# Kernel optimization log

Hardware: AMD Instinct MI355X
Metric: run time of the kernel (lower is better)

## Reference

```python
import jax, jax.numpy as jnp
import numpy as np

N_NODES = 100000
N_EDGES = 3200000
IN_CH, HIDDEN, OUT_CH = 256, 16, 16


def setup_inputs() -> dict:
    key = jax.random.key(0)
    k1, k2, k3, k4, k5, k6 = jax.random.split(key, 6)
    x = jax.random.normal(k1, (N_NODES, IN_CH), dtype=jnp.float32)
    edge_index = jax.random.randint(k2, (2, N_EDGES), 0, N_NODES, dtype=jnp.int64)
    W1 = jax.random.normal(k3, (IN_CH, HIDDEN), dtype=jnp.float32) * (1.0 / np.sqrt(IN_CH))
    b1 = jax.random.normal(k4, (HIDDEN,), dtype=jnp.float32) * 0.01
    W2 = jax.random.normal(k5, (HIDDEN, OUT_CH), dtype=jnp.float32) * (1.0 / np.sqrt(HIDDEN))
    b2 = jax.random.normal(k6, (OUT_CH,), dtype=jnp.float32) * 0.01
    return {"x": x, "edge_index": edge_index, "W1": W1, "b1": b1, "W2": W2, "b2": b2}


def gcn_layer(x, edge_index, W, b):
    # Linear projection: [N, in] @ [in, out] + b
    h = x @ W + b
    source, target = edge_index[0], edge_index[1]
    n = x.shape[0]
    # degree of target nodes (in-degree), symmetric normalization (Kipf & Welling 2017)
    deg = jax.ops.segment_sum(jnp.ones_like(target, dtype=h.dtype), target, num_segments=n)
    deg_inv_sqrt = jnp.where(deg > 0, jax.lax.rsqrt(jnp.maximum(deg, 1.0)), 0.0)
    norm = deg_inv_sqrt[source] * deg_inv_sqrt[target]  # [E]
    # gather-scale-scatter: msg = norm * h[source], aggregated by add at target
    msgs = norm[:, None] * h[source]  # [E, out]
    return jax.ops.segment_sum(msgs, target, num_segments=n)


def reference(x, edge_index, W1, b1, W2, b2):
    h = jax.nn.sigmoid(gcn_layer(x, edge_index, W1, b1))
    return jax.nn.sigmoid(gcn_layer(h, edge_index, W2, b2))
```

## Files before the change

kernel.cpp:

```cpp
#include <hip/hip_runtime.h>
#include <hip/hip_bf16.h>

#define IN_CH 256
#define HID 16
#define BS 256
#define CAP 9216
#define CHUNK 4096
#define PBLK 512
#define EPT (CHUNK/PBLK)
#define SORT_CAP CAP

typedef __attribute__((ext_vector_type(8))) short bf16x8;
typedef __attribute__((ext_vector_type(8))) short short8;
typedef __attribute__((ext_vector_type(4))) float floatx4;

static __device__ __forceinline__ short f2bf(float f) {
    __hip_bfloat16 h = __float2bfloat16(f);
    return *reinterpret_cast<short*>(&h);
}

static __device__ __forceinline__ void acc8(float* a, uint4 v) {
    unsigned w;
    w = v.x;
    a[0] += __uint_as_float(w << 16);
    a[1] += __uint_as_float(w & 0xffff0000u);
    w = v.y;
    a[2] += __uint_as_float(w << 16);
    a[3] += __uint_as_float(w & 0xffff0000u);
    w = v.z;
    a[4] += __uint_as_float(w << 16);
    a[5] += __uint_as_float(w & 0xffff0000u);
    w = v.w;
    a[6] += __uint_as_float(w << 16);
    a[7] += __uint_as_float(w & 0xffff0000u);
}

__global__ __launch_bounds__(PBLK) void k_part(
        const int* __restrict__ src, const int* __restrict__ tgt,
        int* __restrict__ gcursor, unsigned int* __restrict__ csr, int E, int nbuk) {
    __shared__ int lcount[512];
    __shared__ int gspan[512];
    int t = threadIdx.x;
    int base = blockIdx.x * CHUNK;

    lcount[t] = 0;
    __syncthreads();

    int ebuk[EPT], eofs[EPT];
    unsigned epk[EPT];
#pragma unroll
    for (int k = 0; k < EPT; k++) {
        int e = base + t + k * PBLK;
        if (e < E) {
            int s  = __builtin_nontemporal_load(src + e);
            int tg = __builtin_nontemporal_load(tgt + e);
            ebuk[k] = tg >> 8;
            epk[k] = ((unsigned)s << 8) | (unsigned)(tg & 255);
            eofs[k] = atomicAdd(&lcount[ebuk[k]], 1);
        } else {
            ebuk[k] = -1;
        }
    }
    __syncthreads();
    if (t < nbuk) {
        int c = lcount[t];
        if (c > 0) gspan[t] = atomicAdd(&gcursor[t], c);
    }
    __syncthreads();
#pragma unroll
    for (int k = 0; k < EPT; k++) {
        if (ebuk[k] >= 0) {
            int pos = gspan[ebuk[k]] + eofs[k];
            if (pos < CAP)
                csr[(size_t)ebuk[k] * CAP + pos] = epk[k];
        }
    }
}

__global__ __launch_bounds__(512) void k_sort(
        const unsigned int* __restrict__ csr, const int* __restrict__ gcursor,
        int* __restrict__ csr2, int* __restrict__ rowptr,
        int* __restrict__ deg, float* __restrict__ dis, int N) {
    __shared__ int lcnt[256];
    __shared__ int lscan[256];
    __shared__ int ssrc[SORT_CAP];
    int t = threadIdx.x, b = blockIdx.x;
    int start = b * CAP;
    int cnt = min(gcursor[b], CAP);
    int end = start + cnt;

    if (t < 256) lcnt[t] = 0;
    __syncthreads();
    for (int p = start + t; p < end; p += 512) atomicAdd(&lcnt[csr[p] & 255], 1);
    __syncthreads();
    int d = 0;
    if (t < 256) { d = lcnt[t]; lscan[t] = d; }
    __syncthreads();
    for (int off = 1; off < 256; off <<= 1) {
        int a = 0;
        if (t < 256 && t >= off) a = lscan[t - off];
        __syncthreads();
        if (t < 256) lscan[t] += a;
        __syncthreads();
    }
    if (t < 256) {
        int excl = lscan[t] - d;
        int n = b * BS + t;
        if (n < N) {
            rowptr[n] = start + excl;
            deg[n] = d;
            dis[n] = (d > 0) ? rsqrtf((float)d) : 0.0f;
        }
        lcnt[t] = excl;
    }
    __syncthreads();
    for (int p = start + t; p < end; p += 512) {
        unsigned pk = csr[p];
        int pos = atomicAdd(&lcnt[pk & 255], 1);
        ssrc[pos] = (int)(pk >> 8);
    }
    __syncthreads();
    for (int i = t; i < cnt; i += 512) csr2[start + i] = ssrc[i];
}

__global__ void k_gemm1(const float* __restrict__ x,
                        const float* __restrict__ W1,
                        const float* __restrict__ b1,
                        const float* __restrict__ dis,
                        short* __restrict__ h1, int N) {
    int lane = threadIdx.x & 63;
    int wave = threadIdx.x >> 6;
    int tile = blockIdx.x * 4 + wave;
    int nb = tile * 16;
    if (nb >= N) return;

    int mc = lane & 15;
    int q  = lane >> 4;

    bf16x8 bfrag[8];
#pragma unroll
    for (int kb = 0; kb < 8; kb++) {
#pragma unroll
        for (int j = 0; j < 8; j++) {
            bfrag[kb][j] = f2bf(W1[(kb * 32 + q * 8 + j) * HID + mc]);
        }
    }

    const float* xrow = x + (size_t)(nb + mc) * IN_CH;
    floatx4 acc = {0.f, 0.f, 0.f, 0.f};
#pragma unroll
    for (int kb = 0; kb < 8; kb++) {
        const floatx4* p = (const floatx4*)(xrow + kb * 32 + q * 8);
        floatx4 v0 = __builtin_nontemporal_load(p);
        floatx4 v1 = __builtin_nontemporal_load(p + 1);
        bf16x8 afrag;
#pragma unroll
        for (int j = 0; j < 4; j++) {
            afrag[j]     = f2bf(v0[j]);
            afrag[j + 4] = f2bf(v1[j]);
        }
        acc = __builtin_amdgcn_mfma_f32_16x16x32_bf16(afrag, bfrag[kb], acc, 0, 0, 0);
    }

    float bias = b1[mc];
#pragma unroll
    for (int r = 0; r < 4; r++) {
        int node = nb + q * 4 + r;
        if (node < N) {
            h1[(size_t)node * HID + mc] = f2bf((acc[r] + bias) * dis[node]);
        }
    }
}

__global__ __launch_bounds__(256) void k_agg_mid(
        const short* __restrict__ h1, const int* __restrict__ csr2,
        const int* __restrict__ rowptr, const int* __restrict__ deg,
        const float* __restrict__ dis,
        const float* __restrict__ W2, const float* __restrict__ b2,
        short* __restrict__ h2, int N) {
    __shared__ float w2s[256];
    __shared__ float b2s[16];
    __shared__ float sv[128][17];
    int t = threadIdx.x;
    w2s[t] = W2[t];
    if (t < 16) b2s[t] = b2[t];
    int nl = t >> 1;
    int cg = t & 1;
    int n = blockIdx.x * 128 + nl;

    float a[8] = {0.f, 0.f, 0.f, 0.f, 0.f, 0.f, 0.f, 0.f};
    float d = 0.f;
    if (n < N) {
        d = dis[n];
        int start = rowptr[n], cnt = deg[n];
        const short* hb = h1 + 8 * cg;
        int i = start, end4 = start + (cnt & ~3), end = start + cnt;
        if (i < end4) {
            int s0 = csr2[i], s1 = csr2[i + 1], s2 = csr2[i + 2], s3 = csr2[i + 3];
            for (;;) {
                uint4 v0 = *(const uint4*)(hb + 16 * (size_t)s0);
                uint4 v1 = *(const uint4*)(hb + 16 * (size_t)s1);
                uint4 v2 = *(const uint4*)(hb + 16 * (size_t)s2);
                uint4 v3 = *(const uint4*)(hb + 16 * (size_t)s3);
                i += 4;
                bool more = (i < end4);
                int n0, n1, n2, n3;
                if (more) { n0 = csr2[i]; n1 = csr2[i + 1]; n2 = csr2[i + 2]; n3 = csr2[i + 3]; }
                acc8(a, v0); acc8(a, v1); acc8(a, v2); acc8(a, v3);
                if (!more) break;
                s0 = n0; s1 = n1; s2 = n2; s3 = n3;
            }
        }
        for (; i < end; i++) {
            uint4 v = *(const uint4*)(hb + 16 * (size_t)csr2[i]);
            acc8(a, v);
        }
    }
#pragma unroll
    for (int j = 0; j < 8; j++)
        sv[nl][8 * cg + j] = 1.0f / (1.0f + __expf(-d * a[j]));
    __syncthreads();
    if (n < N) {
        float o[8];
#pragma unroll
        for (int j = 0; j < 8; j++) o[j] = b2s[8 * cg + j];
#pragma unroll
        for (int k = 0; k < 16; k++) {
            float s = sv[nl][k];
#pragma unroll
            for (int j = 0; j < 8; j++) o[j] += s * w2s[k * 16 + 8 * cg + j];
        }
        short8 pk;
#pragma unroll
        for (int j = 0; j < 8; j++) pk[j] = f2bf(o[j] * d);
        *(short8*)(h2 + 16 * (size_t)n + 8 * cg) = pk;
    }
}

__global__ __launch_bounds__(256) void k_agg_out(
        const short* __restrict__ h2, const int* __restrict__ csr2,
        const int* __restrict__ rowptr, const int* __restrict__ deg,
        const float* __restrict__ dis, float* __restrict__ out, int N) {
    int t = threadIdx.x;
    int nl = t >> 1;
    int cg = t & 1;
    int n = blockIdx.x * 128 + nl;
    if (n >= N) return;
    float d = dis[n];
    int start = rowptr[n], cnt = deg[n];
    float a[8] = {0.f, 0.f, 0.f, 0.f, 0.f, 0.f, 0.f, 0.f};
    const short* hb = h2 + 8 * cg;
    int i = start, end4 = start + (cnt & ~3), end = start + cnt;
    if (i < end4) {
        int s0 = csr2[i], s1 = csr2[i + 1], s2 = csr2[i + 2], s3 = csr2[i + 3];
        for (;;) {
            uint4 v0 = *(const uint4*)(hb + 16 * (size_t)s0);
            uint4 v1 = *(const uint4*)(hb + 16 * (size_t)s1);
            uint4 v2 = *(const uint4*)(hb + 16 * (size_t)s2);
            uint4 v3 = *(const uint4*)(hb + 16 * (size_t)s3);
            i += 4;
            bool more = (i < end4);
            int n0, n1, n2, n3;
            if (more) { n0 = csr2[i]; n1 = csr2[i + 1]; n2 = csr2[i + 2]; n3 = csr2[i + 3]; }
            acc8(a, v0); acc8(a, v1); acc8(a, v2); acc8(a, v3);
            if (!more) break;
            s0 = n0; s1 = n1; s2 = n2; s3 = n3;
        }
    }
    for (; i < end; i++) {
        uint4 v = *(const uint4*)(hb + 16 * (size_t)csr2[i]);
        acc8(a, v);
    }
    floatx4 o0, o1;
#pragma unroll
    for (int j = 0; j < 4; j++) {
        o0[j] = 1.0f / (1.0f + __expf(-d * a[j]));
        o1[j] = 1.0f / (1.0f + __expf(-d * a[j + 4]));
    }
    float* op = out + 16 * (size_t)n + 8 * cg;
    *(floatx4*)op = o0;
    *(floatx4*)(op + 4) = o1;
}

extern "C" void kernel_launch(void* const* d_in, const int* in_sizes, int n_in,
                              void* d_out, int out_size, void* d_ws, size_t ws_size,
                              hipStream_t stream) {
    const float* x  = (const float*)d_in[0];
    const int*   ei = (const int*)d_in[1];
    const float* W1 = (const float*)d_in[2];
    const float* b1 = (const float*)d_in[3];
    const float* W2 = (const float*)d_in[4];
    const float* b2 = (const float*)d_in[5];
    float* out = (float*)d_out;

    int N = in_sizes[0] / IN_CH;
    int E = in_sizes[1] / 2;
    const int* src = ei;
    const int* tgt = ei + E;

    int NBUK = (N + BS - 1) / BS;

    char* ws = (char*)d_ws;
    auto align256 = [](size_t v) { return (v + 255) & ~(size_t)255; };
    size_t off = 0;
    int*          gcursor = (int*)(ws + off);          off += align256(512 * sizeof(int));
    unsigned int* csr     = (unsigned int*)(ws + off); off += align256((size_t)NBUK * CAP * sizeof(unsigned int));
    int*          csr2    = (int*)(ws + off);          off += align256((size_t)NBUK * CAP * sizeof(int));
    int*          rowptr  = (int*)(ws + off);          off += align256((size_t)N * sizeof(int));
    int*          deg     = (int*)(ws + off);          off += align256((size_t)N * sizeof(int));
    float*        dis     = (float*)(ws + off);        off += align256((size_t)N * sizeof(float));
    short*        h1      = (short*)(ws + off);        off += align256((size_t)N * HID * sizeof(short));
    short*        h2      = (short*)(ws + off);        off += align256((size_t)N * HID * sizeof(short));

    int grid_part = (E + CHUNK - 1) / CHUNK;
    int grid_g1   = ((N + 15) / 16 + 3) / 4;
    int grid_ag   = (N + 127) / 128;

    hipMemsetAsync(gcursor, 0, 512 * sizeof(int), stream);
    k_part   <<<grid_part, PBLK, 0, stream>>>(src, tgt, gcursor, csr, E, NBUK);
    k_sort   <<<NBUK, 512, 0, stream>>>(csr, gcursor, csr2, rowptr, deg, dis, N);
    k_gemm1  <<<grid_g1, 256, 0, stream>>>(x, W1, b1, dis, h1, N);
    k_agg_mid<<<grid_ag, 256, 0, stream>>>(h1, csr2, rowptr, deg, dis, W2, b2, h2, N);
    k_agg_out<<<grid_ag, 256, 0, stream>>>(h2, csr2, rowptr, deg, dis, out, N);
}
```

Baseline: 285.9 us.

## Fuse first-layer GEMM into the per-bucket sort kernel

Merges the x@W1 MFMA projection into the sort kernel, so each 256-node bucket block computes its nodes' h1 rows right after it derives their degree normalisation. The normalisation factors are taken from shared memory instead of a global dis reload, and one kernel launch disappears. The cost is a larger block that does sorting and a 100 MB x stream in sequence, a launch-bounds change that may limit registers, and less parallelism for the GEMM phase (8 waves per 256 nodes).

```diff
diff --git a/kernel.cpp b/kernel.cpp
--- a/kernel.cpp
+++ b/kernel.cpp
@@ -77,12 +77,16 @@
     }
 }
 
-__global__ __launch_bounds__(512) void k_sort(
+__global__ __launch_bounds__(512, 4) void k_sortgemm(
         const unsigned int* __restrict__ csr, const int* __restrict__ gcursor,
+        const float* __restrict__ x, const float* __restrict__ W1,
+        const float* __restrict__ b1,
         int* __restrict__ csr2, int* __restrict__ rowptr,
-        int* __restrict__ deg, float* __restrict__ dis, int N) {
+        int* __restrict__ deg, float* __restrict__ dis,
+        short* __restrict__ h1, int N) {
     __shared__ int lcnt[256];
     __shared__ int lscan[256];
+    __shared__ float sdis[256];
     __shared__ int ssrc[SORT_CAP];
     int t = threadIdx.x, b = blockIdx.x;
     int start = b * CAP;
@@ -106,10 +110,12 @@
     if (t < 256) {
         int excl = lscan[t] - d;
         int n = b * BS + t;
+        float dv = (d > 0) ? rsqrtf((float)d) : 0.0f;
+        sdis[t] = dv;
         if (n < N) {
             rowptr[n] = start + excl;
             deg[n] = d;
-            dis[n] = (d > 0) ? rsqrtf((float)d) : 0.0f;
+            dis[n] = dv;
         }
         lcnt[t] = excl;
     }
@@ -121,53 +127,43 @@
     }
     __syncthreads();
     for (int i = t; i < cnt; i += 512) csr2[start + i] = ssrc[i];
-}
-
-__global__ void k_gemm1(const float* __restrict__ x,
-                        const float* __restrict__ W1,
-                        const float* __restrict__ b1,
-                        const float* __restrict__ dis,
-                        short* __restrict__ h1, int N) {
-    int lane = threadIdx.x & 63;
-    int wave = threadIdx.x >> 6;
-    int tile = blockIdx.x * 4 + wave;
-    int nb = tile * 16;
-    if (nb >= N) return;
-
-    int mc = lane & 15;
-    int q  = lane >> 4;
-
-    bf16x8 bfrag[8];
-#pragma unroll
-    for (int kb = 0; kb < 8; kb++) {
-#pragma unroll
-        for (int j = 0; j < 8; j++) {
-            bfrag[kb][j] = f2bf(W1[(kb * 32 + q * 8 + j) * HID + mc]);
-        }
-    }
-
-    const float* xrow = x + (size_t)(nb + mc) * IN_CH;
-    floatx4 acc = {0.f, 0.f, 0.f, 0.f};
-#pragma unroll
-    for (int kb = 0; kb < 8; kb++) {
-        const floatx4* p = (const floatx4*)(xrow + kb * 32 + q * 8);
-        floatx4 v0 = __builtin_nontemporal_load(p);
-        floatx4 v1 = __builtin_nontemporal_load(p + 1);
-        bf16x8 afrag;
-#pragma unroll
-        for (int j = 0; j < 4; j++) {
-            afrag[j]     = f2bf(v0[j]);
-            afrag[j + 4] = f2bf(v1[j]);
-        }
-        acc = __builtin_amdgcn_mfma_f32_16x16x32_bf16(afrag, bfrag[kb], acc, 0, 0, 0);
-    }
-
-    float bias = b1[mc];
-#pragma unroll
-    for (int r = 0; r < 4; r++) {
-        int node = nb + q * 4 + r;
-        if (node < N) {
-            h1[(size_t)node * HID + mc] = f2bf((acc[r] + bias) * dis[node]);
+
+    {
+        int lane = t & 63, wave = t >> 6;
+        int mc = lane & 15, q = lane >> 4;
+        bf16x8 bfrag[8];
+#pragma unroll
+        for (int kb = 0; kb < 8; kb++) {
+#pragma unroll
+            for (int j = 0; j < 8; j++)
+                bfrag[kb][j] = f2bf(W1[(kb * 32 + q * 8 + j) * HID + mc]);
+        }
+        float bias = b1[mc];
+#pragma unroll
+        for (int r2 = 0; r2 < 2; r2++) {
+            int nb = b * BS + (wave * 2 + r2) * 16;
+            if (nb < N) {
+                const float* xrow = x + (size_t)(nb + mc) * IN_CH;
+                floatx4 acc = {0.f, 0.f, 0.f, 0.f};
+#pragma unroll
+                for (int kb = 0; kb < 8; kb++) {
+                    const floatx4* p = (const floatx4*)(xrow + kb * 32 + q * 8);
+                    floatx4 v0 = __builtin_nontemporal_load(p);
+                    floatx4 v1 = __builtin_nontemporal_load(p + 1);
+                    bf16x8 afrag;
+#pragma unroll
+                    for (int j = 0; j < 4; j++) {
+                        afrag[j]     = f2bf(v0[j]);
+                        afrag[j + 4] = f2bf(v1[j]);
+                    }
+                    acc = __builtin_amdgcn_mfma_f32_16x16x32_bf16(afrag, bfrag[kb], acc, 0, 0, 0);
+                }
+#pragma unroll
+                for (int r = 0; r < 4; r++) {
+                    int node = nb + q * 4 + r;
+                    h1[(size_t)node * HID + mc] = f2bf((acc[r] + bias) * sdis[node - b * BS]);
+                }
+            }
         }
     }
 }
@@ -313,13 +309,12 @@
     short*        h2      = (short*)(ws + off);        off += align256((size_t)N * HID * sizeof(short));
 
     int grid_part = (E + CHUNK - 1) / CHUNK;
-    int grid_g1   = ((N + 15) / 16 + 3) / 4;
     int grid_ag   = (N + 127) / 128;
 
     hipMemsetAsync(gcursor, 0, 512 * sizeof(int), stream);
-    k_part   <<<grid_part, PBLK, 0, stream>>>(src, tgt, gcursor, csr, E, NBUK);
-    k_sort   <<<NBUK, 512, 0, stream>>>(csr, gcursor, csr2, rowptr, deg, dis, N);
-    k_gemm1  <<<grid_g1, 256, 0, stream>>>(x, W1, b1, dis, h1, N);
-    k_agg_mid<<<grid_ag, 256, 0, stream>>>(h1, csr2, rowptr, deg, dis, W2, b2, h2, N);
-    k_agg_out<<<grid_ag, 256, 0, stream>>>(h2, csr2, rowptr, deg, dis, out, N);
-}
+    k_part    <<<grid_part, PBLK, 0, stream>>>(src, tgt, gcursor, csr, E, NBUK);
+    k_sortgemm<<<NBUK, 512, 0, stream>>>(csr, gcursor, x, W1, b1,
+                                         csr2, rowptr, deg, dis, h1, N);
+    k_agg_mid <<<grid_ag, 256, 0, stream>>>(h1, csr2, rowptr, deg, dis, W2, b2, h2, N);
+    k_agg_out <<<grid_ag, 256, 0, stream>>>(h2, csr2, rowptr, deg, dis, out, N);
+}
```

New measurement: 285.6 us. No clear change (-0.1%).
